# Performance work log

Measured on AMD Instinct MI355X. Metric: run time of the kernel, lower is better.

Reference implementation:

```python
import jax, jax.numpy as jnp
import numpy as np

B, S, D = 4, 2048, 1024
H, DK, DV = 16, 64, 64  # heads, key_size, size_per_head
NEG = 1000000000.0


def setup_inputs() -> dict:
    key = jax.random.key(0)
    ks = jax.random.split(key, 8)
    scale = 1.0 / np.sqrt(D)
    return {
        "q": jax.random.normal(ks[0], (B, S, D), jnp.float32),
        "k": jax.random.normal(ks[1], (B, S, D), jnp.float32),
        "v": jax.random.normal(ks[2], (B, S, D), jnp.float32),
        "v_mask": jax.random.randint(ks[3], (B, S), 0, 2).astype(jnp.float32),
        "q_mask": jax.random.randint(ks[4], (B, S), 0, 2).astype(jnp.float32),
        "Wq": jax.random.normal(ks[5], (D, H * DK), jnp.float32) * scale,
        "Wk": jax.random.normal(ks[6], (D, H * DK), jnp.float32) * scale,
        "Wv": jax.random.normal(ks[7], (D, H * DV), jnp.float32) * scale,
    }


def reference(q, k, v, v_mask, q_mask, Wq, Wk, Wv):
    b, sq, _ = q.shape
    sk = k.shape[1]
    # projections + head split: [B, H, S, Dh]
    qw = (q @ Wq).reshape(b, sq, H, DK).transpose(0, 2, 1, 3)
    kw = (k @ Wk).reshape(b, sk, H, DK).transpose(0, 2, 1, 3)
    vw = (v @ Wv).reshape(b, sk, H, DV).transpose(0, 2, 1, 3)
    # scaled dot-product scores [B, H, Sq, Sk]
    a = jnp.einsum("bhqd,bhkd->bhqk", qw, kw) / jnp.sqrt(jnp.float32(DK))
    # additive kv-mask (v_mask over key axis)
    a = a - (1.0 - v_mask)[:, None, None, :] * NEG
    # causal (mask_right=True): subtract 1e9 on strictly-upper triangle
    causal = jnp.triu(jnp.ones((sq, sk), jnp.float32), k=1) * NEG
    a = a - causal[None, None]
    a = jax.nn.softmax(a, axis=-1)
    o = jnp.einsum("bhqk,bhkd->bhqd", a, vw)
    o = o.transpose(0, 2, 1, 3).reshape(b, sq, H * DV)
    # multiplicative query mask on output
    return o * q_mask[:, :, None]
```

## Files before the change

kernel.cpp:

```cpp
#include <hip/hip_runtime.h>

#define S_LEN 2048
#define NHEAD 16

typedef float f32x4 __attribute__((ext_vector_type(4)));
typedef __bf16 bf16x8 __attribute__((ext_vector_type(8)));
typedef __bf16 bf16x4 __attribute__((ext_vector_type(4)));

#define AS1 __attribute__((address_space(1)))
#define AS3 __attribute__((address_space(3)))

__device__ __forceinline__ void gl2lds16(const void* g, void* l) {
    __builtin_amdgcn_global_load_lds((const AS1 unsigned int*)g,
                                     (AS3 unsigned int*)l, 16, 0, 0);
}
__device__ __forceinline__ void wb_leave4() {
    asm volatile("s_waitcnt vmcnt(4)\n\ts_barrier" ::: "memory");
}
__device__ __forceinline__ void wb_drain() {
    asm volatile("s_waitcnt vmcnt(0)\n\ts_barrier" ::: "memory");
}

__global__ __launch_bounds__(256) void cast_swizzle_kernel(
    const float* __restrict__ q, const float* __restrict__ k,
    const float* __restrict__ v, __bf16* __restrict__ out)
{
    int gid = blockIdx.x * 256 + threadIdx.x;
    int z   = gid >> 20;
    int rem = gid & 1048575;
    int r   = rem >> 7;
    int c   = rem & 127;
    const float* src = (z == 0 ? q : z == 1 ? k : v) + (size_t)r * 1024 + c * 8;
    float4 a = *(const float4*)src;
    float4 b = *(const float4*)(src + 4);
    bf16x8 t;
    t[0] = (__bf16)a.x; t[1] = (__bf16)a.y; t[2] = (__bf16)a.z; t[3] = (__bf16)a.w;
    t[4] = (__bf16)b.x; t[5] = (__bf16)b.y; t[6] = (__bf16)b.z; t[7] = (__bf16)b.w;
    int cp = (c & ~7) | ((c ^ r) & 7);
    *(bf16x8*)(out + (size_t)z * 8388608 + (size_t)r * 1024 + cp * 8) = t;
}

__global__ __launch_bounds__(256) void transpose_cast_kernel(
    const float* __restrict__ W0, const float* __restrict__ W1,
    const float* __restrict__ W2, __bf16* __restrict__ Wt)
{
    int z = blockIdx.z;
    const float* W = (z == 0 ? W0 : z == 1 ? W1 : W2);
    __bf16* out = Wt + (size_t)z * 1048576;
    __shared__ float tile[32][33];
    int bx = blockIdx.x, by = blockIdx.y;
    int tid = threadIdx.x;
    int tx = tid & 31, ty = tid >> 5;
    for (int i = 0; i < 32; i += 8)
        tile[ty + i][tx] = W[(size_t)(by * 32 + ty + i) * 1024 + bx * 32 + tx];
    __syncthreads();
    if (tid < 128) {
        int nl = tid >> 2, kc = tid & 3;
        int n = bx * 32 + nl;
        int kbase = by * 32 + kc * 8;
        bf16x8 t;
        for (int j = 0; j < 8; j++) t[j] = (__bf16)tile[kc * 8 + j][nl];
        int cp = ((kbase >> 3) ^ n) & 7;
        *(bf16x8*)(out + (size_t)n * 1024 + (kbase & ~63) + cp * 8) = t;
    }
}

__global__ __launch_bounds__(256, 3) void proj_gemm_kernel(
    const __bf16* __restrict__ Abf, const __bf16* __restrict__ Wt,
    __bf16* __restrict__ qw, __bf16* __restrict__ kw, __bf16* __restrict__ vt)
{
    int z = blockIdx.z;
    const __bf16* A = Abf + (size_t)z * 8388608;
    const __bf16* B = Wt + (size_t)z * 1048576;
    __shared__ __align__(16) char smem[49152];

    int tid = threadIdx.x;
    int bm = blockIdx.x, bn = blockIdx.y;
    int wave = tid >> 6, lane = tid & 63;
    int wm = (wave >> 1) * 64, wn = (wave & 1) * 64;
    int lrow = lane & 15;
    int q4 = lane >> 4;
    int l4r = lane >> 2, j4 = lane & 3;

    auto pf = [&](int kb) {
        int sl = kb % 3;
        int k0 = kb * 32;
        int segbyte = (k0 >> 6) * 128;
        int cbase = (k0 & 32) >> 3;
        for (int i = 0; i < 2; i++) {
            int r = wave * 32 + i * 16 + l4r;
            int cl = j4 ^ ((r >> 1) & 3);
            int phys = ((cbase + cl) ^ r) & 7;
            gl2lds16((const char*)A + (size_t)(bm * 128 + r) * 2048 + segbyte + phys * 16,
                     smem + sl * 8192 + wave * 2048 + i * 1024);
            gl2lds16((const char*)B + (size_t)(bn * 128 + r) * 2048 + segbyte + phys * 16,
                     smem + 24576 + sl * 8192 + wave * 2048 + i * 1024);
        }
    };

    f32x4 zero = {0.f, 0.f, 0.f, 0.f};
    f32x4 acc[4][4];
    for (int mt = 0; mt < 4; mt++)
        for (int nt = 0; nt < 4; nt++) acc[mt][nt] = zero;

    pf(0); pf(1);
    __syncthreads();
    for (int kb = 0; kb < 32; kb++) {
        if (kb == 31) wb_drain(); else wb_leave4();
        if (kb + 2 < 32) pf(kb + 2);
        int sA = (kb % 3) * 8192, sB = 24576 + (kb % 3) * 8192;
        bf16x8 af[4], bfv[4];
        for (int mt = 0; mt < 4; mt++) {
            int r = wm + mt * 16 + lrow;
            af[mt] = *(const bf16x8*)(smem + sA + r * 64 + (q4 ^ ((r >> 1) & 3)) * 16);
        }
        for (int nt = 0; nt < 4; nt++) {
            int r = wn + nt * 16 + lrow;
            bfv[nt] = *(const bf16x8*)(smem + sB + r * 64 + (q4 ^ ((r >> 1) & 3)) * 16);
        }
        for (int mt = 0; mt < 4; mt++)
            for (int nt = 0; nt < 4; nt++)
                acc[mt][nt] = __builtin_amdgcn_mfma_f32_16x16x32_bf16(
                    af[mt], bfv[nt], acc[mt][nt], 0, 0, 0);
    }
    __syncthreads();
    __bf16* T = (__bf16*)smem;

    float oscale = (z == 0) ? 0.125f : 1.0f;
    int rowoff = q4 * 4;
    int b = bm >> 4;
    int s_base = (bm & 15) * 128;
    if (z < 2) {
        for (int mt = 0; mt < 4; mt++) {
            for (int nt = 0; nt < 4; nt++) {
                int n_local = wn + nt * 16 + lrow;
                int hl = n_local >> 6, d = n_local & 63;
                for (int reg = 0; reg < 4; reg++) {
                    int s_local = wm + mt * 16 + rowoff + reg;
                    int s = s_base + s_local;
                    int dp = (d & 7) | ((((d >> 3) ^ s) & 7) << 3);
                    T[s_local * 136 + hl * 64 + dp] = (__bf16)(acc[mt][nt][reg] * oscale);
                }
            }
        }
        __syncthreads();
        char* gq = (char*)(z == 0 ? qw : kw);
        for (int i = 0; i < 8; i++) {
            int id = tid + i * 256;
            int hl = id >> 10, r = (id >> 3) & 127, j = id & 7;
            float4 val = *(float4*)((char*)T + r * 272 + hl * 128 + j * 16);
            *(float4*)(gq + ((size_t)((b * 16 + bn * 2 + hl) * 2048) + s_base + r) * 128
                          + j * 16) = val;
        }
    } else {
        for (int mt = 0; mt < 4; mt++) {
            int s0 = wm + mt * 16 + rowoff;
            int seg = s0 >> 6, j0 = s0 & 63;
            for (int nt = 0; nt < 4; nt++) {
                int n_local = wn + nt * 16 + lrow;
                int d = n_local & 63;
                int hi = ((j0 >> 3) ^ d) & 7;
                bf16x4 pk;
                for (int reg = 0; reg < 4; reg++) pk[reg] = (__bf16)acc[mt][nt][reg];
                *(bf16x4*)&T[n_local * 136 + seg * 64 + hi * 8 + (j0 & 7)] = pk;
            }
        }
        __syncthreads();
        char* gv = (char*)vt;
        for (int i = 0; i < 8; i++) {
            int id = tid + i * 256;
            int nl = id >> 4, j = id & 15;
            int hl = nl >> 6, dv = nl & 63;
            float4 val = *(float4*)((char*)T + nl * 272 + j * 16);
            *(float4*)(gv + (((size_t)((b * 16 + bn * 2 + hl) * 64 + dv)) * 2048 + s_base) * 2
                          + j * 16) = val;
        }
    }
}

__global__ __launch_bounds__(256, 2) void attn_kernel(
    const __bf16* __restrict__ QW, const __bf16* __restrict__ KW,
    const __bf16* __restrict__ VT, const float* __restrict__ v_mask,
    const float* __restrict__ q_mask, float* __restrict__ out)
{
    int lin = blockIdx.x + (blockIdx.y << 4);
    int xcd = lin & 7;
    int jj  = lin >> 3;
    int bh  = (xcd << 3) + (jj >> 4);
    int bx  = jj & 15;
    int b = bh >> 4, h = bh & 15;

    __shared__ __align__(16) char lds[40960];
    char* Kb0 = lds;
    char* Vb0 = lds + 16384;
    char* Pw  = lds + 32768;

    int tid = threadIdx.x;
    int wave = tid >> 6, lane = tid & 63;
    int mloc = lane & 15, q4 = lane >> 4;
    int rowoff = q4 * 4, x7 = mloc & 7;
    char* Pme = Pw + wave * 2048;

    const char* Krow = (const char*)KW + (size_t)bh * 2048 * 128;
    const char* Vrow = (const char*)VT + (size_t)bh * 64 * 4096;
    const float* vmrow = v_mask + (size_t)b * 2048;

    int id0 = tid, id1 = tid + 256;

    auto stage = [&](int kb, int slot) {
        char* kd = Kb0 + slot * 8192;
        char* vd = Vb0 + slot * 8192;
        gl2lds16(Krow + (size_t)(kb * 64 + (id0 >> 3)) * 128 + (id0 & 7) * 16,
                 kd + id0 * 16);
        gl2lds16(Krow + (size_t)(kb * 64 + (id1 >> 3)) * 128 + (id1 & 7) * 16,
                 kd + id1 * 16);
        gl2lds16(Vrow + (size_t)(id0 >> 3) * 4096 + (size_t)kb * 128 + (id0 & 7) * 16,
                 vd + id0 * 16);
        gl2lds16(Vrow + (size_t)(id1 >> 3) * 4096 + (size_t)kb * 128 + (id1 & 7) * 16,
                 vd + id1 * 16);
    };

    f32x4 zero = {0.f, 0.f, 0.f, 0.f};

    for (int p = 0; p < 2; p++) {
        int qb = p ? (31 - bx) : bx;
        const char* Qrow = (const char*)QW +
                           ((size_t)bh * 2048 + qb * 64 + wave * 16) * 128;
        bf16x8 qfr[2];
        for (int kc = 0; kc < 2; kc++)
            qfr[kc] = *(const bf16x8*)(Qrow + mloc * 128 + (((kc * 4 + q4) ^ x7) << 4));

        stage(0, 0);

        f32x4 o_acc[4];
        for (int nt = 0; nt < 4; nt++) o_acc[nt] = zero;
        float lt = 0.f;

        for (int kb = 0; kb <= qb; kb++) {
            int slot = kb & 1;
            float4 vm4[4];
            for (int m = 0; m < 4; m++)
                vm4[m] = *(const float4*)(vmrow + kb * 64 + m * 16 + rowoff);
            if (kb < qb) {
                stage(kb + 1, slot ^ 1);
                wb_leave4();
            } else {
                wb_drain();
            }
            const char* Kls = Kb0 + slot * 8192;
            const char* Vls = Vb0 + slot * 8192;

            f32x4 sacc[4];
            for (int m = 0; m < 4; m++) sacc[m] = zero;
            for (int kc = 0; kc < 2; kc++) {
                bf16x8 kfr[4];
                for (int m = 0; m < 4; m++)
                    kfr[m] = *(const bf16x8*)(Kls + (m * 16 + mloc) * 128 +
                                              (((kc * 4 + q4) ^ x7) << 4));
                for (int m = 0; m < 4; m++)
                    sacc[m] = __builtin_amdgcn_mfma_f32_16x16x32_bf16(
                        kfr[m], qfr[kc], sacc[m], 0, 0, 0);
            }
            for (int m = 0; m < 4; m++) {
                float pen[4];
                pen[0] = fmaf(1.0f - vm4[m].x, 1.0e9f, 12.0f);
                pen[1] = fmaf(1.0f - vm4[m].y, 1.0e9f, 12.0f);
                pen[2] = fmaf(1.0f - vm4[m].z, 1.0e9f, 12.0f);
                pen[3] = fmaf(1.0f - vm4[m].w, 1.0e9f, 12.0f);
                float pv[4];
                for (int reg = 0; reg < 4; reg++)
                    pv[reg] = __expf(sacc[m][reg] - pen[reg]);
                if (kb == qb)
                    for (int reg = 0; reg < 4; reg++)
                        if (m * 16 + rowoff + reg > wave * 16 + mloc) pv[reg] = 0.f;
                lt += (pv[0] + pv[1]) + (pv[2] + pv[3]);
                bf16x4 pk;
                for (int reg = 0; reg < 4; reg++) pk[reg] = (__bf16)pv[reg];
                *(bf16x4*)(Pme + mloc * 128 +
                           (((m * 2 + (q4 >> 1)) ^ x7) << 4) + (q4 & 1) * 8) = pk;
            }
            for (int kc = 0; kc < 2; kc++) {
                bf16x8 afr = *(const bf16x8*)(Pme + mloc * 128 +
                                              (((kc * 4 + q4) ^ x7) << 4));
                bf16x8 vfr[4];
                for (int nt = 0; nt < 4; nt++)
                    vfr[nt] = *(const bf16x8*)(Vls + (nt * 16 + mloc) * 128 +
                                               (((kc * 4 + q4) ^ x7) << 4));
                for (int nt = 0; nt < 4; nt++)
                    o_acc[nt] = __builtin_amdgcn_mfma_f32_16x16x32_bf16(
                        afr, vfr[nt], o_acc[nt], 0, 0, 0);
            }
            __syncthreads();
        }

        lt += __shfl_xor(lt, 16);
        lt += __shfl_xor(lt, 32);

        if (__any(lt == 0.0f)) {
            float l2 = 0.f;
            bool degrow = (lt == 0.0f);
            int qrow = qb * 64 + wave * 16 + mloc;
            for (int kb2 = 0; kb2 < 32; kb2++) {
                bf16x8 vfr[4][2];
                for (int nt = 0; nt < 4; nt++)
                    for (int kc = 0; kc < 2; kc++)
                        vfr[nt][kc] = *(const bf16x8*)(Vrow +
                            (size_t)(nt * 16 + mloc) * 4096 +
                            kb2 * 128 + (((kc * 4 + q4) ^ x7) << 4));
                for (int kc = 0; kc < 2; kc++) {
                    const float* vmp = vmrow + kb2 * 64 + kc * 32 + q4 * 8;
                    float4 va = *(const float4*)vmp;
                    float4 vb4 = *(const float4*)(vmp + 4);
                    float vmj[8] = {va.x, va.y, va.z, va.w,
                                    vb4.x, vb4.y, vb4.z, vb4.w};
                    int kg0 = kb2 * 64 + kc * 32 + q4 * 8;
                    bf16x8 af;
                    float cnt = 0.f;
                    for (int j = 0; j < 8; j++) {
                        float ind = degrow ? ((kg0 + j <= qrow) ? 1.0f : vmj[j]) : 0.0f;
                        af[j] = (__bf16)ind;
                        cnt += ind;
                    }
                    l2 += cnt;
                    for (int nt = 0; nt < 4; nt++)
                        o_acc[nt] = __builtin_amdgcn_mfma_f32_16x16x32_bf16(
                            af, vfr[nt][kc], o_acc[nt], 0, 0, 0);
                }
            }
            l2 += __shfl_xor(l2, 16);
            l2 += __shfl_xor(l2, 32);
            if (degrow) lt = l2;
        }

        float sc[4];
        for (int reg = 0; reg < 4; reg++) {
            float lq = __shfl(lt, rowoff + reg);
            sc[reg] = q_mask[b * 2048 + qb * 64 + wave * 16 + rowoff + reg] / lq;
        }
        for (int nt = 0; nt < 4; nt++)
            for (int reg = 0; reg < 4; reg++)
                out[((size_t)(b * 2048 + qb * 64 + wave * 16 + rowoff + reg)) * 1024 +
                    h * 64 + nt * 16 + mloc] = o_acc[nt][reg] * sc[reg];
    }
}

extern "C" void kernel_launch(void* const* d_in, const int* in_sizes, int n_in,
                              void* d_out, int out_size, void* d_ws, size_t ws_size,
                              hipStream_t stream)
{
    const float* q      = (const float*)d_in[0];
    const float* k      = (const float*)d_in[1];
    const float* v      = (const float*)d_in[2];
    const float* v_mask = (const float*)d_in[3];
    const float* q_mask = (const float*)d_in[4];
    const float* Wq     = (const float*)d_in[5];
    const float* Wk     = (const float*)d_in[6];
    const float* Wv     = (const float*)d_in[7];
    float* out = (float*)d_out;

    __bf16* Abf = (__bf16*)d_ws;
    __bf16* Wt  = Abf + (size_t)3 * 8388608;
    __bf16* qw  = Wt + (size_t)3 * 1048576;
    __bf16* kw  = qw + (size_t)8388608;
    __bf16* vt  = kw + (size_t)8388608;

    cast_swizzle_kernel<<<12288, 256, 0, stream>>>(q, k, v, Abf);
    transpose_cast_kernel<<<dim3(32, 32, 3), 256, 0, stream>>>(Wq, Wk, Wv, Wt);
    proj_gemm_kernel<<<dim3(64, 8, 3), 256, 0, stream>>>(Abf, Wt, qw, kw, vt);
    attn_kernel<<<dim3(16, 64), 256, 0, stream>>>(qw, kw, vt, v_mask, q_mask, out);
}
```

Baseline: 308.2 us.

## Load K/V fragments directly to registers and software-pipeline QK with PV

Drops the shared-memory double buffering of K and V tiles, which used global_load_lds plus block barriers. Each wave now loads its K and V fragments straight from global memory into registers, one tile ahead. The loop is skewed so that the softmax and PV product for tile j-1 overlap with the QK product for tile j. This removes the __syncthreads per tile and cuts LDS use to the per-wave P buffer. In exchange, every wave redundantly fetches the full K/V tiles from global/L2 and register pressure rises from the prefetched fragments.

```diff
diff --git a/kernel.cpp b/kernel.cpp
--- a/kernel.cpp
+++ b/kernel.cpp
@@ -190,35 +190,16 @@
     int bx  = jj & 15;
     int b = bh >> 4, h = bh & 15;
 
-    __shared__ __align__(16) char lds[40960];
-    char* Kb0 = lds;
-    char* Vb0 = lds + 16384;
-    char* Pw  = lds + 32768;
-
+    __shared__ __align__(16) char lds[8192];
     int tid = threadIdx.x;
     int wave = tid >> 6, lane = tid & 63;
     int mloc = lane & 15, q4 = lane >> 4;
     int rowoff = q4 * 4, x7 = mloc & 7;
-    char* Pme = Pw + wave * 2048;
+    char* Pme = lds + wave * 2048;
 
     const char* Krow = (const char*)KW + (size_t)bh * 2048 * 128;
     const char* Vrow = (const char*)VT + (size_t)bh * 64 * 4096;
     const float* vmrow = v_mask + (size_t)b * 2048;
-
-    int id0 = tid, id1 = tid + 256;
-
-    auto stage = [&](int kb, int slot) {
-        char* kd = Kb0 + slot * 8192;
-        char* vd = Vb0 + slot * 8192;
-        gl2lds16(Krow + (size_t)(kb * 64 + (id0 >> 3)) * 128 + (id0 & 7) * 16,
-                 kd + id0 * 16);
-        gl2lds16(Krow + (size_t)(kb * 64 + (id1 >> 3)) * 128 + (id1 & 7) * 16,
-                 kd + id1 * 16);
-        gl2lds16(Vrow + (size_t)(id0 >> 3) * 4096 + (size_t)kb * 128 + (id0 & 7) * 16,
-                 vd + id0 * 16);
-        gl2lds16(Vrow + (size_t)(id1 >> 3) * 4096 + (size_t)kb * 128 + (id1 & 7) * 16,
-                 vd + id1 * 16);
-    };
 
     f32x4 zero = {0.f, 0.f, 0.f, 0.f};
 
@@ -230,67 +211,102 @@
         for (int kc = 0; kc < 2; kc++)
             qfr[kc] = *(const bf16x8*)(Qrow + mloc * 128 + (((kc * 4 + q4) ^ x7) << 4));
 
-        stage(0, 0);
+        bf16x8 kcur[2][4];
+        for (int kc = 0; kc < 2; kc++)
+            for (int m = 0; m < 4; m++)
+                kcur[kc][m] = *(const bf16x8*)(Krow +
+                    (size_t)(m * 16 + mloc) * 128 + (((kc * 4 + q4) ^ x7) << 4));
+        float4 vmP[4];
+        for (int m = 0; m < 4; m++)
+            vmP[m] = *(const float4*)(vmrow + m * 16 + rowoff);
 
         f32x4 o_acc[4];
         for (int nt = 0; nt < 4; nt++) o_acc[nt] = zero;
+        f32x4 sacc[4];
         float lt = 0.f;
-
-        for (int kb = 0; kb <= qb; kb++) {
-            int slot = kb & 1;
-            float4 vm4[4];
-            for (int m = 0; m < 4; m++)
-                vm4[m] = *(const float4*)(vmrow + kb * 64 + m * 16 + rowoff);
-            if (kb < qb) {
-                stage(kb + 1, slot ^ 1);
-                wb_leave4();
-            } else {
-                wb_drain();
-            }
-            const char* Kls = Kb0 + slot * 8192;
-            const char* Vls = Vb0 + slot * 8192;
-
-            f32x4 sacc[4];
+        bf16x8 vprev[2][4];
+
+        for (int j = 0; j <= qb; j++) {
+            bf16x8 knext[2][4], vnext[2][4];
+            bool hasK = (j + 1 <= qb);
+            if (hasK)
+                for (int kc = 0; kc < 2; kc++)
+                    for (int m = 0; m < 4; m++)
+                        knext[kc][m] = *(const bf16x8*)(Krow +
+                            (size_t)((j + 1) * 64 + m * 16 + mloc) * 128 +
+                            (((kc * 4 + q4) ^ x7) << 4));
+            for (int kc = 0; kc < 2; kc++)
+                for (int nt = 0; nt < 4; nt++)
+                    vnext[kc][nt] = *(const bf16x8*)(Vrow +
+                        (size_t)(nt * 16 + mloc) * 4096 + (size_t)j * 128 +
+                        (((kc * 4 + q4) ^ x7) << 4));
+
+            if (j >= 1) {
+                for (int m = 0; m < 4; m++) {
+                    float pen[4];
+                    pen[0] = fmaf(1.0f - vmP[m].x, 1.0e9f, 12.0f);
+                    pen[1] = fmaf(1.0f - vmP[m].y, 1.0e9f, 12.0f);
+                    pen[2] = fmaf(1.0f - vmP[m].z, 1.0e9f, 12.0f);
+                    pen[3] = fmaf(1.0f - vmP[m].w, 1.0e9f, 12.0f);
+                    float pv[4];
+                    for (int reg = 0; reg < 4; reg++)
+                        pv[reg] = __expf(sacc[m][reg] - pen[reg]);
+                    lt += (pv[0] + pv[1]) + (pv[2] + pv[3]);
+                    bf16x4 pk;
+                    for (int reg = 0; reg < 4; reg++) pk[reg] = (__bf16)pv[reg];
+                    *(bf16x4*)(Pme + mloc * 128 +
+                               (((m * 2 + (q4 >> 1)) ^ x7) << 4) + (q4 & 1) * 8) = pk;
+                }
+                for (int m = 0; m < 4; m++)
+                    vmP[m] = *(const float4*)(vmrow + j * 64 + m * 16 + rowoff);
+            }
+
             for (int m = 0; m < 4; m++) sacc[m] = zero;
-            for (int kc = 0; kc < 2; kc++) {
-                bf16x8 kfr[4];
-                for (int m = 0; m < 4; m++)
-                    kfr[m] = *(const bf16x8*)(Kls + (m * 16 + mloc) * 128 +
-                                              (((kc * 4 + q4) ^ x7) << 4));
+            for (int kc = 0; kc < 2; kc++)
                 for (int m = 0; m < 4; m++)
                     sacc[m] = __builtin_amdgcn_mfma_f32_16x16x32_bf16(
-                        kfr[m], qfr[kc], sacc[m], 0, 0, 0);
-            }
-            for (int m = 0; m < 4; m++) {
-                float pen[4];
-                pen[0] = fmaf(1.0f - vm4[m].x, 1.0e9f, 12.0f);
-                pen[1] = fmaf(1.0f - vm4[m].y, 1.0e9f, 12.0f);
-                pen[2] = fmaf(1.0f - vm4[m].z, 1.0e9f, 12.0f);
-                pen[3] = fmaf(1.0f - vm4[m].w, 1.0e9f, 12.0f);
-                float pv[4];
-                for (int reg = 0; reg < 4; reg++)
-                    pv[reg] = __expf(sacc[m][reg] - pen[reg]);
-                if (kb == qb)
-                    for (int reg = 0; reg < 4; reg++)
-                        if (m * 16 + rowoff + reg > wave * 16 + mloc) pv[reg] = 0.f;
-                lt += (pv[0] + pv[1]) + (pv[2] + pv[3]);
-                bf16x4 pk;
-                for (int reg = 0; reg < 4; reg++) pk[reg] = (__bf16)pv[reg];
-                *(bf16x4*)(Pme + mloc * 128 +
-                           (((m * 2 + (q4 >> 1)) ^ x7) << 4) + (q4 & 1) * 8) = pk;
-            }
-            for (int kc = 0; kc < 2; kc++) {
-                bf16x8 afr = *(const bf16x8*)(Pme + mloc * 128 +
-                                              (((kc * 4 + q4) ^ x7) << 4));
-                bf16x8 vfr[4];
-                for (int nt = 0; nt < 4; nt++)
-                    vfr[nt] = *(const bf16x8*)(Vls + (nt * 16 + mloc) * 128 +
-                                               (((kc * 4 + q4) ^ x7) << 4));
-                for (int nt = 0; nt < 4; nt++)
-                    o_acc[nt] = __builtin_amdgcn_mfma_f32_16x16x32_bf16(
-                        afr, vfr[nt], o_acc[nt], 0, 0, 0);
-            }
-            __syncthreads();
+                        kcur[kc][m], qfr[kc], sacc[m], 0, 0, 0);
+
+            if (j >= 1) {
+                for (int kc = 0; kc < 2; kc++) {
+                    bf16x8 afr = *(const bf16x8*)(Pme + mloc * 128 +
+                                                  (((kc * 4 + q4) ^ x7) << 4));
+                    for (int nt = 0; nt < 4; nt++)
+                        o_acc[nt] = __builtin_amdgcn_mfma_f32_16x16x32_bf16(
+                            afr, vprev[kc][nt], o_acc[nt], 0, 0, 0);
+                }
+            }
+
+            if (hasK)
+                for (int kc = 0; kc < 2; kc++)
+                    for (int m = 0; m < 4; m++) kcur[kc][m] = knext[kc][m];
+            for (int kc = 0; kc < 2; kc++)
+                for (int nt = 0; nt < 4; nt++) vprev[kc][nt] = vnext[kc][nt];
+        }
+
+        for (int m = 0; m < 4; m++) {
+            float pen[4];
+            pen[0] = fmaf(1.0f - vmP[m].x, 1.0e9f, 12.0f);
+            pen[1] = fmaf(1.0f - vmP[m].y, 1.0e9f, 12.0f);
+            pen[2] = fmaf(1.0f - vmP[m].z, 1.0e9f, 12.0f);
+            pen[3] = fmaf(1.0f - vmP[m].w, 1.0e9f, 12.0f);
+            float pv[4];
+            for (int reg = 0; reg < 4; reg++)
+                pv[reg] = __expf(sacc[m][reg] - pen[reg]);
+            for (int reg = 0; reg < 4; reg++)
+                if (m * 16 + rowoff + reg > wave * 16 + mloc) pv[reg] = 0.f;
+            lt += (pv[0] + pv[1]) + (pv[2] + pv[3]);
+            bf16x4 pk;
+            for (int reg = 0; reg < 4; reg++) pk[reg] = (__bf16)pv[reg];
+            *(bf16x4*)(Pme + mloc * 128 +
+                       (((m * 2 + (q4 >> 1)) ^ x7) << 4) + (q4 & 1) * 8) = pk;
+        }
+        for (int kc = 0; kc < 2; kc++) {
+            bf16x8 afr = *(const bf16x8*)(Pme + mloc * 128 +
+                                          (((kc * 4 + q4) ^ x7) << 4));
+            for (int nt = 0; nt < 4; nt++)
+                o_acc[nt] = __builtin_amdgcn_mfma_f32_16x16x32_bf16(
+                    afr, vprev[kc][nt], o_acc[nt], 0, 0, 0);
         }
 
         lt += __shfl_xor(lt, 16);
@@ -316,9 +332,9 @@
                     int kg0 = kb2 * 64 + kc * 32 + q4 * 8;
                     bf16x8 af;
                     float cnt = 0.f;
-                    for (int j = 0; j < 8; j++) {
-                        float ind = degrow ? ((kg0 + j <= qrow) ? 1.0f : vmj[j]) : 0.0f;
-                        af[j] = (__bf16)ind;
+                    for (int jx = 0; jx < 8; jx++) {
+                        float ind = degrow ? ((kg0 + jx <= qrow) ? 1.0f : vmj[jx]) : 0.0f;
+                        af[jx] = (__bf16)ind;
                         cnt += ind;
                     }
                     l2 += cnt;
```

Result: slower. 384.9 us (+24.9%).
